# Kernel tuning notes

Hardware: AMD Instinct MI355X
Metric: run time of the kernel (lower is better)

Reference implementation:

```python
import jax, jax.numpy as jnp
import numpy as np

IGNORE_INDEX = -100
BETA = 0.1


def _seq_logps(x, W, b, tgt):
    """Per-sequence summed target log-probs. x:(B,S,H) W:(V,H) b:(V,) tgt:(B,S) -> (B,)"""
    logits = jnp.einsum('bsh,vh->bsv', x, W) + b           # (B,S,V)
    lsm = jax.nn.log_softmax(logits, axis=-1)
    tok_logp = jnp.take_along_axis(lsm, tgt[..., None].astype(jnp.int32), axis=-1)[..., 0]
    mask = (tgt != IGNORE_INDEX).astype(x.dtype)
    return (tok_logp * mask).sum(axis=-1)


def setup_inputs() -> dict:
    key = jax.random.key(0)
    ks = jax.random.split(key, 10)
    B, S, H, V = 2, 512, 2048, 32000
    sc = 1.0 / np.sqrt(H)
    return {
        'x_chosen': jax.random.normal(ks[0], (B, S, H), jnp.float32),
        'x_rejected': jax.random.normal(ks[1], (B, S, H), jnp.float32),
        'ref_x_chosen': jax.random.normal(ks[2], (B, S, H), jnp.float32),
        'ref_x_rejected': jax.random.normal(ks[3], (B, S, H), jnp.float32),
        'weight': jax.random.normal(ks[4], (V, H), jnp.float32) * sc,
        'bias': jnp.zeros((V,), jnp.float32),
        'ref_weight': jax.random.normal(ks[5], (V, H), jnp.float32) * sc,
        'ref_bias': jnp.zeros((V,), jnp.float32),
        'target_chosen': jax.random.randint(ks[6], (B, S), 0, V, jnp.int32),
        'target_rejected': jax.random.randint(ks[7], (B, S), 0, V, jnp.int32),
    }


def reference(x_chosen, x_rejected, ref_x_chosen, ref_x_rejected,
              weight, bias, ref_weight, ref_bias,
              target_chosen, target_rejected):
    B = x_chosen.shape[0]  # number of preference pairs (chosen batch size)

    # policy log-probs
    chosen_logps = _seq_logps(x_chosen, weight, bias, target_chosen)
    rejected_logps = _seq_logps(x_rejected, weight, bias, target_rejected)

    # reference model log-probs (no grad in the original: computed under no_grad)
    ref_chosen_logps = jax.lax.stop_gradient(_seq_logps(ref_x_chosen, ref_weight, ref_bias, target_chosen))
    ref_rejected_logps = jax.lax.stop_gradient(_seq_logps(ref_x_rejected, ref_weight, ref_bias, target_rejected))

    # DPO sigmoid loss
    pi_logratios = chosen_logps - rejected_logps
    ref_logratios = ref_chosen_logps - ref_rejected_logps
    logits_diff = BETA * (pi_logratios - ref_logratios)
    loss = -jax.nn.log_sigmoid(logits_diff).sum() / B

    chosen_rewards = BETA * (chosen_logps - ref_chosen_logps)
    rejected_rewards = BETA * (rejected_logps - ref_rejected_logps)
    reward_margin = (chosen_rewards - rejected_rewards).mean()
    reward_acc = (chosen_rewards > rejected_rewards).astype(jnp.float32).mean()
    policy_nll_loss = jnp.zeros((), x_chosen.dtype)  # compute_nll_loss=False

    return (loss, chosen_rewards.mean(), rejected_rewards.mean(),
            reward_margin, reward_acc, policy_nll_loss)
```

## Files before the change

### kernel.cpp

```cpp
#include <hip/hip_runtime.h>
#include <hip/hip_bf16.h>
#include <math.h>

#define DIM_H 2048
#define VOCAB 32000
#define BK 32

typedef _Float16 half8v __attribute__((ext_vector_type(8)));
typedef _Float16 half4v __attribute__((ext_vector_type(4)));
typedef float floatx4 __attribute__((ext_vector_type(4)));

__device__ __forceinline__ void async_copy16(void* lds, const void* g) {
  __builtin_amdgcn_global_load_lds(
      (const __attribute__((address_space(1))) void*)g,
      (__attribute__((address_space(3))) void*)lds,
      16, 0, 0);
}

__global__ void cvt_f32_f16(const float* __restrict__ src, _Float16* __restrict__ dst, long n) {
  long i = ((long)blockIdx.x * blockDim.x + threadIdx.x) * 4;
  if (i + 3 < n) {
    const float4 v = *(const float4*)(src + i);
    half4v h;
    h.x = (_Float16)v.x; h.y = (_Float16)v.y; h.z = (_Float16)v.z; h.w = (_Float16)v.w;
    *(half4v*)(dst + i) = h;
  }
}

__global__ void prep(const float* __restrict__ xc, const float* __restrict__ xr,
                     const float* __restrict__ rxc, const float* __restrict__ rxr,
                     const float* __restrict__ W, _Float16* __restrict__ X16,
                     _Float16* __restrict__ W16,
                     const int* __restrict__ tc, const int* __restrict__ tr,
                     int* __restrict__ tgt) {
  const long b = blockIdx.x;
  if (b < 64000) {
    const long i = (b * 256 + threadIdx.x) * 4;
    const float4 v = *(const float4*)(W + i);
    half4v h;
    h.x = (_Float16)v.x; h.y = (_Float16)v.y; h.z = (_Float16)v.z; h.w = (_Float16)v.w;
    *(half4v*)(W16 + i) = h;
  } else if (b < 72192) {
    const long t = ((b - 64000) * 256 + threadIdx.x) * 4;
    const int seg = (int)(t >> 21);
    const long off = t & ((1L << 21) - 1);
    const float* src = seg == 0 ? xc : seg == 1 ? xr : seg == 2 ? rxc : rxr;
    const float4 v = *(const float4*)(src + off);
    half4v h;
    h.x = (_Float16)v.x; h.y = (_Float16)v.y; h.z = (_Float16)v.z; h.w = (_Float16)v.w;
    *(half4v*)(X16 + t) = h;
  } else {
    const int t = (int)(b - 72192) * 256 + threadIdx.x;
    if (t < 2048) tgt[t] = (t < 1024) ? tc[t] : tr[t - 1024];
  }
}

__global__ __launch_bounds__(256, 4)
void gemm_lse(const _Float16* __restrict__ X, const _Float16* __restrict__ W,
              const float* __restrict__ bias, const int* __restrict__ tgt,
              float* __restrict__ sumexp, float* __restrict__ tgtlogit) {
  __shared__ _Float16 sA[128 * BK];
  __shared__ _Float16 sB[128 * BK];

  const int tid = threadIdx.x;
  const int m0 = blockIdx.x << 7;
  const int n0 = blockIdx.y << 7;

  const int ldr = tid >> 2;
  const int ldc = (((tid & 3) ^ ((tid >> 3) & 3)) << 3);
  const _Float16* gA = X + (size_t)(m0 + ldr) * DIM_H + ldc;
  const _Float16* gB = W + (size_t)(n0 + ldr) * DIM_H + ldc;
  _Float16* lA = sA + tid * 8;
  _Float16* lB = sB + tid * 8;

  const int lane = tid & 63;
  const int w = tid >> 6;
  const int wm = (w & 1) << 6;
  const int wn = (w >> 1) << 6;
  const int l15 = lane & 15;
  const int q = lane >> 4;
  const int swz = (l15 >> 1) & 3;

  int aoff[4], boff[4];
#pragma unroll
  for (int i = 0; i < 4; ++i) {
    aoff[i] = (wm + i * 16 + l15) * BK + ((q ^ swz) << 3);
    boff[i] = (wn + i * 16 + l15) * BK + ((q ^ swz) << 3);
  }

  floatx4 acc[4][4];
#pragma unroll
  for (int mi = 0; mi < 4; ++mi)
#pragma unroll
    for (int ni = 0; ni < 4; ++ni)
      acc[mi][ni] = 0.0f;

  for (int kt = 0; kt < DIM_H; kt += BK) {
    __syncthreads();
    async_copy16(lA,            gA + kt);
    async_copy16(lA + 64 * BK,  gA + kt + (size_t)64 * DIM_H);
    async_copy16(lB,            gB + kt);
    async_copy16(lB + 64 * BK,  gB + kt + (size_t)64 * DIM_H);
    __syncthreads();

    half8v af[4], bf[4];
#pragma unroll
    for (int i = 0; i < 4; ++i) {
      af[i] = *(const half8v*)(sA + aoff[i]);
      bf[i] = *(const half8v*)(sB + boff[i]);
    }
#pragma unroll
    for (int mi = 0; mi < 4; ++mi)
#pragma unroll
      for (int ni = 0; ni < 4; ++ni)
        acc[mi][ni] = __builtin_amdgcn_mfma_f32_16x16x32_f16(af[mi], bf[ni], acc[mi][ni], 0, 0, 0);
  }

  float bv[4];
#pragma unroll
  for (int ni = 0; ni < 4; ++ni) bv[ni] = bias[n0 + wn + ni * 16 + l15];

#pragma unroll
  for (int mi = 0; mi < 4; ++mi) {
#pragma unroll
    for (int reg = 0; reg < 4; ++reg) {
      const int row = m0 + wm + mi * 16 + q * 4 + reg;
      const int tv = tgt[row];
      float s = 0.f;
#pragma unroll
      for (int ni = 0; ni < 4; ++ni) {
        const float lg = acc[mi][ni][reg] + bv[ni];
        s += __expf(lg);
        if (tv == n0 + wn + ni * 16 + l15) tgtlogit[row] = lg;
      }
      s += __shfl_xor(s, 1, 16);
      s += __shfl_xor(s, 2, 16);
      s += __shfl_xor(s, 4, 16);
      s += __shfl_xor(s, 8, 16);
      if (l15 == 0) atomicAdd(&sumexp[row], s);
    }
  }
}

__global__ void dpo_reduce(const float* __restrict__ sumexp, const float* __restrict__ tgtlogit,
                           const int* __restrict__ tgt, float* __restrict__ out) {
  __shared__ float r[8];
  const int tid = threadIdx.x;
  const int j = tid >> 6;
  const int lane = tid & 63;
  const int g = j >> 1, b = j & 1;
  float sum = 0.f;
  for (int s = lane; s < 512; s += 64) {
    const int slot = g * 1024 + b * 512 + s;
    const int tv = tgt[slot & 2047];
    if (tv != -100) sum += tgtlogit[slot] - logf(sumexp[slot]);
  }
#pragma unroll
  for (int m = 1; m < 64; m <<= 1) sum += __shfl_xor(sum, m, 64);
  if (lane == 0) r[j] = sum;
  __syncthreads();
  if (tid == 0) {
    const float beta = 0.1f;
    float pc[2] = {r[0], r[1]}, pr[2] = {r[2], r[3]};
    float rc[2] = {r[4], r[5]}, rr[2] = {r[6], r[7]};
    float loss = 0.f, cr[2], rj[2];
    for (int bb = 0; bb < 2; ++bb) {
      float d = beta * ((pc[bb] - pr[bb]) - (rc[bb] - rr[bb]));
      float ls = fminf(d, 0.f) - log1pf(expf(-fabsf(d)));
      loss += -ls;
      cr[bb] = beta * (pc[bb] - rc[bb]);
      rj[bb] = beta * (pr[bb] - rr[bb]);
    }
    out[0] = loss * 0.5f;
    out[1] = 0.5f * (cr[0] + cr[1]);
    out[2] = 0.5f * (rj[0] + rj[1]);
    out[3] = 0.5f * ((cr[0] - rj[0]) + (cr[1] - rj[1]));
    out[4] = 0.5f * ((cr[0] > rj[0] ? 1.f : 0.f) + (cr[1] > rj[1] ? 1.f : 0.f));
    out[5] = 0.f;
  }
}

extern "C" void kernel_launch(void* const* d_in, const int* in_sizes, int n_in,
                              void* d_out, int out_size, void* d_ws, size_t ws_size,
                              hipStream_t stream) {
  const float* x_c   = (const float*)d_in[0];
  const float* x_r   = (const float*)d_in[1];
  const float* rx_c  = (const float*)d_in[2];
  const float* rx_r  = (const float*)d_in[3];
  const float* Wt    = (const float*)d_in[4];
  const float* bias  = (const float*)d_in[5];
  const float* rWt   = (const float*)d_in[6];
  const float* rbias = (const float*)d_in[7];
  const int*   tc    = (const int*)d_in[8];
  const int*   tr    = (const int*)d_in[9];
  float* out = (float*)d_out;

  char* ws = (char*)d_ws;
  const size_t W16_B = (size_t)VOCAB * DIM_H * 2;
  const size_t X16_B = (size_t)4096 * DIM_H * 2;
  _Float16* W16   = (_Float16*)ws;
  _Float16* X16   = (_Float16*)(ws + W16_B);
  float*    sume  = (float*)(ws + W16_B + X16_B);
  float*    tlog  = (float*)(ws + W16_B + X16_B + 16384);
  int*      tgt   = (int*)  (ws + W16_B + X16_B + 32768);

  hipMemsetAsync(sume, 0, 32768, stream);

  prep<<<72200, 256, 0, stream>>>(x_c, x_r, rx_c, rx_r, Wt, X16, W16, tc, tr, tgt);

  const long nx = 1024L * DIM_H;
  const long nw = (long)VOCAB * DIM_H;
  dim3 ggrid(2048 / 128, VOCAB / 128);

  gemm_lse<<<ggrid, 256, 0, stream>>>(X16, W16, bias, tgt, sume, tlog);

  cvt_f32_f16<<<(unsigned)(nw / 4 / 256), 256, 0, stream>>>(rWt, W16, nw);
  gemm_lse<<<ggrid, 256, 0, stream>>>(X16 + 2 * nx, W16, rbias, tgt, sume + 2048, tlog + 2048);

  dpo_reduce<<<1, 512, 0, stream>>>(sume, tlog, tgt, out);
}
```

Measured before the change: 1.201 ms.

## Rewrite GEMM-LSE as 256x256 tile, double-buffered pipelined MFMA kernel

The fused GEMM+log-sum-exp kernel moves from a 128x128 tile with BK=32 and a single LDS buffer to a 256x256 tile with BK=64 and double-buffered LDS. Global-to-LDS async copies for later k-steps are interleaved with MFMA phases, using explicit waitcnt, barriers and setprio. Blocks are remapped over a 1D grid so consecutive blocks group by N tile for L2 reuse. The aim is to hide load latency, cut barrier overhead per FLOP and raise arithmetic intensity, at the cost of more LDS and registers and lower occupancy.

```diff
diff --git a/kernel.cpp b/kernel.cpp
--- a/kernel.cpp
+++ b/kernel.cpp
@@ -4,7 +4,10 @@
 
 #define DIM_H 2048
 #define VOCAB 32000
-#define BK 32
+#define BM 256
+#define BN 256
+#define BKT 64
+#define NT (DIM_H / BKT)
 
 typedef _Float16 half8v __attribute__((ext_vector_type(8)));
 typedef _Float16 half4v __attribute__((ext_vector_type(4)));
@@ -55,83 +58,170 @@
   }
 }
 
-__global__ __launch_bounds__(256, 4)
+__global__ __launch_bounds__(512, 2)
 void gemm_lse(const _Float16* __restrict__ X, const _Float16* __restrict__ W,
               const float* __restrict__ bias, const int* __restrict__ tgt,
               float* __restrict__ sumexp, float* __restrict__ tgtlogit) {
-  __shared__ _Float16 sA[128 * BK];
-  __shared__ _Float16 sB[128 * BK];
+  __shared__ _Float16 sA[2][BM][BKT];
+  __shared__ _Float16 sB[2][BN][BKT];
 
   const int tid = threadIdx.x;
-  const int m0 = blockIdx.x << 7;
-  const int n0 = blockIdx.y << 7;
-
-  const int ldr = tid >> 2;
-  const int ldc = (((tid & 3) ^ ((tid >> 3) & 3)) << 3);
-  const _Float16* gA = X + (size_t)(m0 + ldr) * DIM_H + ldc;
-  const _Float16* gB = W + (size_t)(n0 + ldr) * DIM_H + ldc;
-  _Float16* lA = sA + tid * 8;
-  _Float16* lB = sB + tid * 8;
+
+  const int lin = blockIdx.x;
+  const int nl  = (lin & 7) * 125 + (lin >> 3);
+  const int m0  = (nl & 7) << 8;
+  const int n0  = (nl >> 3) << 8;
+
+  const int srow   = tid >> 3;
+  const int schunk = (tid & 7) ^ (srow & 7);
+  const _Float16* gA = X + (size_t)(m0 + srow) * DIM_H + schunk * 8;
+  const _Float16* gB = W + (size_t)(n0 + srow) * DIM_H + schunk * 8;
+  _Float16* lA = &sA[0][0][0] + tid * 8;
+  _Float16* lB = &sB[0][0][0] + tid * 8;
+
+#define STG_A(buf, tt, h) { \
+    const _Float16* g_ = gA + (size_t)((h) * 128) * DIM_H + (tt) * BKT; \
+    _Float16* l_ = lA + (buf) * 16384 + (h) * 8192; \
+    async_copy16(l_, g_); \
+    async_copy16(l_ + 4096, g_ + (size_t)64 * DIM_H); }
+#define STG_B(buf, tt, h) { \
+    const _Float16* g_ = gB + (size_t)((h) * 128) * DIM_H + (tt) * BKT; \
+    _Float16* l_ = lB + (buf) * 16384 + (h) * 8192; \
+    async_copy16(l_, g_); \
+    async_copy16(l_ + 4096, g_ + (size_t)64 * DIM_H); }
 
   const int lane = tid & 63;
-  const int w = tid >> 6;
-  const int wm = (w & 1) << 6;
-  const int wn = (w >> 1) << 6;
+  const int w   = tid >> 6;
+  const int wm  = (w >> 2) * 128;
+  const int wn  = (w & 3) * 64;
   const int l15 = lane & 15;
-  const int q = lane >> 4;
-  const int swz = (l15 >> 1) & 3;
-
-  int aoff[4], boff[4];
-#pragma unroll
-  for (int i = 0; i < 4; ++i) {
-    aoff[i] = (wm + i * 16 + l15) * BK + ((q ^ swz) << 3);
-    boff[i] = (wn + i * 16 + l15) * BK + ((q ^ swz) << 3);
-  }
-
-  floatx4 acc[4][4];
-#pragma unroll
-  for (int mi = 0; mi < 4; ++mi)
-#pragma unroll
-    for (int ni = 0; ni < 4; ++ni)
-      acc[mi][ni] = 0.0f;
-
-  for (int kt = 0; kt < DIM_H; kt += BK) {
-    __syncthreads();
-    async_copy16(lA,            gA + kt);
-    async_copy16(lA + 64 * BK,  gA + kt + (size_t)64 * DIM_H);
-    async_copy16(lB,            gB + kt);
-    async_copy16(lB + 64 * BK,  gB + kt + (size_t)64 * DIM_H);
-    __syncthreads();
-
-    half8v af[4], bf[4];
-#pragma unroll
-    for (int i = 0; i < 4; ++i) {
-      af[i] = *(const half8v*)(sA + aoff[i]);
-      bf[i] = *(const half8v*)(sB + boff[i]);
-    }
-#pragma unroll
-    for (int mi = 0; mi < 4; ++mi)
-#pragma unroll
-      for (int ni = 0; ni < 4; ++ni)
-        acc[mi][ni] = __builtin_amdgcn_mfma_f32_16x16x32_f16(af[mi], bf[ni], acc[mi][ni], 0, 0, 0);
+  const int q   = lane >> 4;
+  const int key = l15 & 7;
+  const int cofs0 = ((q ^ key) & 7) * 8;
+  const int cofs1 = (((4 + q) ^ key) & 7) * 8;
+
+  const _Float16* pA = &sA[0][0][0] + (wm + l15) * BKT;
+  const _Float16* pB = &sB[0][0][0] + (wn + l15) * BKT;
+
+  floatx4 acc[8][4];
+#pragma unroll
+  for (int mf = 0; mf < 8; ++mf)
+#pragma unroll
+    for (int nf = 0; nf < 4; ++nf) acc[mf][nf] = 0.0f;
+
+  STG_A(0, 0, 0); STG_A(0, 0, 1);
+  STG_B(0, 0, 0); STG_B(0, 0, 1);
+  STG_A(1, 1, 0); STG_A(1, 1, 1);
+  asm volatile("s_waitcnt vmcnt(4)" ::: "memory");
+  __builtin_amdgcn_s_barrier();
+
+  for (int t = 0; t < NT; ++t) {
+    const int cur = t & 1;
+    const int nxt = cur ^ 1;
+    const int cb  = cur * 16384;
+
+    half8v af[8][2], b01[2][2], b23[2][2];
+
+#pragma unroll
+    for (int mf = 0; mf < 4; ++mf) {
+      af[mf][0] = *(const half8v*)(pA + cb + mf * 1024 + cofs0);
+      af[mf][1] = *(const half8v*)(pA + cb + mf * 1024 + cofs1);
+    }
+#pragma unroll
+    for (int nf = 0; nf < 2; ++nf) {
+      b01[nf][0] = *(const half8v*)(pB + cb + nf * 1024 + cofs0);
+      b01[nf][1] = *(const half8v*)(pB + cb + nf * 1024 + cofs1);
+    }
+    if (t + 1 < NT) STG_B(nxt, t + 1, 0);
+    __builtin_amdgcn_s_barrier();
+    asm volatile("s_waitcnt lgkmcnt(0)" ::: "memory");
+    __builtin_amdgcn_sched_barrier(0);
+    __builtin_amdgcn_s_setprio(1);
+#pragma unroll
+    for (int mf = 0; mf < 4; ++mf)
+#pragma unroll
+      for (int nf = 0; nf < 2; ++nf) {
+        acc[mf][nf] = __builtin_amdgcn_mfma_f32_16x16x32_f16(af[mf][0], b01[nf][0], acc[mf][nf], 0, 0, 0);
+        acc[mf][nf] = __builtin_amdgcn_mfma_f32_16x16x32_f16(af[mf][1], b01[nf][1], acc[mf][nf], 0, 0, 0);
+      }
+    __builtin_amdgcn_s_setprio(0);
+    __builtin_amdgcn_s_barrier();
+
+#pragma unroll
+    for (int mf = 4; mf < 8; ++mf) {
+      af[mf][0] = *(const half8v*)(pA + cb + mf * 1024 + cofs0);
+      af[mf][1] = *(const half8v*)(pA + cb + mf * 1024 + cofs1);
+    }
+    if (t + 1 < NT) STG_B(nxt, t + 1, 1);
+    __builtin_amdgcn_s_barrier();
+    asm volatile("s_waitcnt lgkmcnt(0)" ::: "memory");
+    __builtin_amdgcn_sched_barrier(0);
+    __builtin_amdgcn_s_setprio(1);
+#pragma unroll
+    for (int mf = 4; mf < 8; ++mf)
+#pragma unroll
+      for (int nf = 0; nf < 2; ++nf) {
+        acc[mf][nf] = __builtin_amdgcn_mfma_f32_16x16x32_f16(af[mf][0], b01[nf][0], acc[mf][nf], 0, 0, 0);
+        acc[mf][nf] = __builtin_amdgcn_mfma_f32_16x16x32_f16(af[mf][1], b01[nf][1], acc[mf][nf], 0, 0, 0);
+      }
+    __builtin_amdgcn_s_setprio(0);
+    __builtin_amdgcn_s_barrier();
+
+#pragma unroll
+    for (int nf = 0; nf < 2; ++nf) {
+      b23[nf][0] = *(const half8v*)(pB + cb + (nf + 2) * 1024 + cofs0);
+      b23[nf][1] = *(const half8v*)(pB + cb + (nf + 2) * 1024 + cofs1);
+    }
+    if (t + 2 < NT) STG_A(cur, t + 2, 0);
+    __builtin_amdgcn_s_barrier();
+    asm volatile("s_waitcnt lgkmcnt(0)" ::: "memory");
+    __builtin_amdgcn_sched_barrier(0);
+    __builtin_amdgcn_s_setprio(1);
+#pragma unroll
+    for (int mf = 0; mf < 4; ++mf)
+#pragma unroll
+      for (int nf = 0; nf < 2; ++nf) {
+        acc[mf][nf + 2] = __builtin_amdgcn_mfma_f32_16x16x32_f16(af[mf][0], b23[nf][0], acc[mf][nf + 2], 0, 0, 0);
+        acc[mf][nf + 2] = __builtin_amdgcn_mfma_f32_16x16x32_f16(af[mf][1], b23[nf][1], acc[mf][nf + 2], 0, 0, 0);
+      }
+    __builtin_amdgcn_s_setprio(0);
+    __builtin_amdgcn_s_barrier();
+
+    if (t + 2 < NT) STG_A(cur, t + 2, 1);
+    if (t < NT - 2) {
+      asm volatile("s_waitcnt vmcnt(4)" ::: "memory");
+    } else if (t == NT - 2) {
+      asm volatile("s_waitcnt vmcnt(0)" ::: "memory");
+    }
+    __builtin_amdgcn_s_barrier();
+    __builtin_amdgcn_s_setprio(1);
+#pragma unroll
+    for (int mf = 4; mf < 8; ++mf)
+#pragma unroll
+      for (int nf = 0; nf < 2; ++nf) {
+        acc[mf][nf + 2] = __builtin_amdgcn_mfma_f32_16x16x32_f16(af[mf][0], b23[nf][0], acc[mf][nf + 2], 0, 0, 0);
+        acc[mf][nf + 2] = __builtin_amdgcn_mfma_f32_16x16x32_f16(af[mf][1], b23[nf][1], acc[mf][nf + 2], 0, 0, 0);
+      }
+    __builtin_amdgcn_s_setprio(0);
+    __builtin_amdgcn_s_barrier();
   }
 
   float bv[4];
 #pragma unroll
-  for (int ni = 0; ni < 4; ++ni) bv[ni] = bias[n0 + wn + ni * 16 + l15];
-
-#pragma unroll
-  for (int mi = 0; mi < 4; ++mi) {
+  for (int nf = 0; nf < 4; ++nf) bv[nf] = bias[n0 + wn + nf * 16 + l15];
+
+#pragma unroll
+  for (int mf = 0; mf < 8; ++mf) {
 #pragma unroll
     for (int reg = 0; reg < 4; ++reg) {
-      const int row = m0 + wm + mi * 16 + q * 4 + reg;
+      const int row = m0 + wm + mf * 16 + q * 4 + reg;
       const int tv = tgt[row];
       float s = 0.f;
 #pragma unroll
-      for (int ni = 0; ni < 4; ++ni) {
-        const float lg = acc[mi][ni][reg] + bv[ni];
+      for (int nf = 0; nf < 4; ++nf) {
+        const float lg = acc[mf][nf][reg] + bv[nf];
         s += __expf(lg);
-        if (tv == n0 + wn + ni * 16 + l15) tgtlogit[row] = lg;
+        if (tv == n0 + wn + nf * 16 + l15) tgtlogit[row] = lg;
       }
       s += __shfl_xor(s, 1, 16);
       s += __shfl_xor(s, 2, 16);
@@ -140,6 +230,8 @@
       if (l15 == 0) atomicAdd(&sumexp[row], s);
     }
   }
+#undef STG_A
+#undef STG_B
 }
 
 __global__ void dpo_reduce(const float* __restrict__ sumexp, const float* __restrict__ tgtlogit,
@@ -210,12 +302,11 @@
 
   const long nx = 1024L * DIM_H;
   const long nw = (long)VOCAB * DIM_H;
-  dim3 ggrid(2048 / 128, VOCAB / 128);
-
-  gemm_lse<<<ggrid, 256, 0, stream>>>(X16, W16, bias, tgt, sume, tlog);
+
+  gemm_lse<<<1000, 512, 0, stream>>>(X16, W16, bias, tgt, sume, tlog);
 
   cvt_f32_f16<<<(unsigned)(nw / 4 / 256), 256, 0, stream>>>(rWt, W16, nw);
-  gemm_lse<<<ggrid, 256, 0, stream>>>(X16 + 2 * nx, W16, rbias, tgt, sume + 2048, tlog + 2048);
+  gemm_lse<<<1000, 512, 0, stream>>>(X16 + 2 * nx, W16, rbias, tgt, sume + 2048, tlog + 2048);
 
   dpo_reduce<<<1, 512, 0, stream>>>(sume, tlog, tgt, out);
 }
```

Result: no change. 1.209 ms (+0.7%).
